# Kernel optimization log

Measured on AMD Instinct MI355X. Metric: run time of the kernel, lower is better.

The kernel has to match this reference:

```python
import jax, jax.numpy as jnp
import numpy as np

OBS, HOR, PD, HID, NH, PROTO = 8, 8, 128, 256, 8, 32
B, N = 8, 4096

def _gelu(x):
    return jax.nn.gelu(x, approximate=False)  # torch nn.GELU default is exact erf

def setup_inputs():
    key = jax.random.key(0)
    ks = iter(jax.random.split(key, 40))
    nrm = lambda shape, s=0.02: jax.random.normal(next(ks), shape, dtype=jnp.float32) * s
    return {
        'obs_points': jax.random.normal(next(ks), (B, N, OBS, 2), dtype=jnp.float32),
        'obs_vis': jax.random.randint(next(ks), (B, N, OBS), 0, 2).astype(bool),
        'rel_xy': jax.random.normal(next(ks), (B, N, 2), dtype=jnp.float32),
        'anchor_obs': jax.random.normal(next(ks), (B, OBS, 2), dtype=jnp.float32),
        'anchor_obs_vel': jax.random.normal(next(ks), (B, OBS, 2), dtype=jnp.float32),
        'semantic_feat': jax.random.normal(next(ks), (B, N, 10), dtype=jnp.float32),
        'ln_w': jnp.ones((OBS * 7,), jnp.float32),
        'ln_b': jnp.zeros((OBS * 7,), jnp.float32),
        'enc_w1': nrm((OBS * 7, PD)), 'enc_b1': jnp.zeros((PD,), jnp.float32),
        'enc_w2': nrm((PD, PD)), 'enc_b2': jnp.zeros((PD,), jnp.float32),
        'time_embed': nrm((HOR, HID)),
        'anchor_w': nrm((OBS * 4, HID)), 'anchor_b': jnp.zeros((HID,), jnp.float32),
        'query_w': nrm((PD, HID)), 'query_b': jnp.zeros((HID,), jnp.float32),
        'in_proj_w': nrm((HID, 3 * HID)), 'in_proj_b': jnp.zeros((3 * HID,), jnp.float32),
        'out_proj_w': nrm((HID, HID)), 'out_proj_b': jnp.zeros((HID,), jnp.float32),
        'ah_w': nrm((HID, 2)), 'ah_b': jnp.zeros((2,), jnp.float32),
        'rh_w1': nrm((HID + PD + 2, HID)), 'rh_b1': jnp.zeros((HID,), jnp.float32),
        'rh_w2': nrm((HID, 2)), 'rh_b2': jnp.zeros((2,), jnp.float32),
        'vh_w1': nrm((HID + PD, HID // 2)), 'vh_b1': jnp.zeros((HID // 2,), jnp.float32),
        'vh_w2': nrm((HID // 2, 1)), 'vh_b2': jnp.zeros((1,), jnp.float32),
        'sh_w': nrm((HID, PROTO)), 'sh_b': jnp.zeros((PROTO,), jnp.float32),
    }

def reference(obs_points, obs_vis, rel_xy, anchor_obs, anchor_obs_vel, semantic_feat,
              ln_w, ln_b, enc_w1, enc_b1, enc_w2, enc_b2, time_embed,
              anchor_w, anchor_b, query_w, query_b, in_proj_w, in_proj_b,
              out_proj_w, out_proj_b, ah_w, ah_b, rh_w1, rh_b1, rh_w2, rh_b2,
              vh_w1, vh_b1, vh_w2, vh_b2, sh_w, sh_b):
    del semantic_feat  # unused, matches original
    Bc, Nc, T, _ = obs_points.shape
    # ---- PointTraceEncoder ----
    vel = jnp.concatenate([jnp.zeros_like(obs_points[:, :, :1]),
                           obs_points[:, :, 1:] - obs_points[:, :, :-1]], axis=2)
    rel = jnp.broadcast_to(rel_xy[:, :, None, :], (Bc, Nc, T, 2))
    feat = jnp.concatenate([obs_points, vel, obs_vis.astype(jnp.float32)[..., None], rel],
                           axis=-1).reshape(Bc, Nc, T * 7)
    mu = feat.mean(-1, keepdims=True)
    var = ((feat - mu) ** 2).mean(-1, keepdims=True)
    x = (feat - mu) / jnp.sqrt(var + 1e-5) * ln_w + ln_b
    point_tokens = _gelu(_gelu(x @ enc_w1 + enc_b1) @ enc_w2 + enc_b2)  # [B,N,PD]
    # ---- queries / memory ----
    anchor_feat = jnp.concatenate([anchor_obs, anchor_obs_vel], -1).reshape(Bc, -1)
    tq = time_embed[None] + (anchor_feat @ anchor_w + anchor_b)[:, None]  # [B,HOR,HID]
    mem = point_tokens @ query_w + query_b  # [B,N,HID]
    # ---- multi-head cross attention ----
    D = tq.shape[-1]; dh = D // NH
    q = tq @ in_proj_w[:, :D] + in_proj_b[:D]
    k = mem @ in_proj_w[:, D:2 * D] + in_proj_b[D:2 * D]
    v = mem @ in_proj_w[:, 2 * D:] + in_proj_b[2 * D:]
    qh = q.reshape(Bc, -1, NH, dh).transpose(0, 2, 1, 3)
    kh = k.reshape(Bc, -1, NH, dh).transpose(0, 2, 1, 3)
    vh = v.reshape(Bc, -1, NH, dh).transpose(0, 2, 1, 3)
    attn = jax.nn.softmax(jnp.einsum('bhqd,bhkd->bhqk', qh, kh) / jnp.sqrt(jnp.float32(dh)), axis=-1)
    o = jnp.einsum('bhqk,bhkd->bhqd', attn, vh).transpose(0, 2, 1, 3).reshape(Bc, -1, D)
    future = o @ out_proj_w + out_proj_b  # [B,HOR,HID]
    # ---- heads ----
    last_anchor = anchor_obs[:, -1]
    anchor_delta = 0.1 * jnp.tanh(future @ ah_w + ah_b)
    anchor_pred = last_anchor[:, None] + jnp.cumsum(anchor_delta, axis=1)  # [B,HOR,2]
    Hq = future.shape[1]
    ft_e = jnp.broadcast_to(future[:, :, None, :], (Bc, Hq, Nc, D))
    pt_e = jnp.broadcast_to(point_tokens[:, None], (Bc, Hq, Nc, point_tokens.shape[-1]))
    rel_e = jnp.broadcast_to(rel_xy[:, None], (Bc, Hq, Nc, 2))
    per_point = jnp.concatenate([ft_e, pt_e, rel_e], axis=-1)  # [B,HOR,N,HID+PD+2]
    residual = 0.1 * jnp.tanh(_gelu(per_point @ rh_w1 + rh_b1) @ rh_w2 + rh_b2)
    pred_points = anchor_pred[:, :, None, :] + residual
    vis_logits = (_gelu(per_point[..., :-2] @ vh_w1 + vh_b1) @ vh_w2 + vh_b2)[..., 0]
    sem_logits = future @ sh_w + sh_b
    return (anchor_pred,
            pred_points.transpose(0, 2, 1, 3),   # [B,N,HOR,2]
            vis_logits.transpose(0, 2, 1),       # [B,N,HOR]
            sem_logits)                           # [B,HOR,PROTO]
```

## Files before the change

### kernel.cpp

```cpp
#include <hip/hip_runtime.h>
#include <math.h>

#define BB 8
#define NN 4096
#define TT 8
#define HORQ 8
#define PD 128
#define HID 256
#define NHD 8
#define DH 32
#define FE 56
#define NC2 16
#define CH2 256

typedef __attribute__((ext_vector_type(8))) short short8;
typedef __attribute__((ext_vector_type(4))) float floatx4;
typedef unsigned short ushort_t;

__device__ __forceinline__ float gelu_fast(float x) {
    float x2 = x * x;
    float y2 = x * fmaf(0.0713551f, x2, 1.5957691f);
    float e = __expf(y2);
    return x - x * __builtin_amdgcn_rcpf(1.f + e);
}

__device__ __forceinline__ float tanh_fast(float x) {
    float e = __expf(2.f * x);
    return 1.f - 2.f * __builtin_amdgcn_rcpf(1.f + e);
}

__device__ __forceinline__ ushort_t f2b(float x) {
    union { float f; unsigned u; } c; c.f = x;
    unsigned r = c.u + 0x7fffu + ((c.u >> 16) & 1u);
    return (ushort_t)(r >> 16);
}
__device__ __forceinline__ float b2f(unsigned hi) {
    union { unsigned u; float f; } c; c.u = hi;
    return c.f;
}

__global__ __launch_bounds__(256) void k_fuse(
    const float* __restrict__ qw, const float* __restrict__ qb,
    const float* __restrict__ ipw, const float* __restrict__ ipb,
    float* __restrict__ Wk, float* __restrict__ Wv,
    float* __restrict__ bk, float* __restrict__ bv)
{
    int j = threadIdx.x;
    int blk = blockIdx.x;
    if (blk < PD) {
        float sk = 0.f, sv = 0.f;
        for (int l = 0; l < HID; l++) {
            float w = qw[blk * HID + l];
            sk += w * ipw[l * 768 + 256 + j];
            sv += w * ipw[l * 768 + 512 + j];
        }
        Wk[blk * HID + j] = sk;
        Wv[blk * HID + j] = sv;
    } else {
        float sk = ipb[256 + j], sv = ipb[512 + j];
        for (int l = 0; l < HID; l++) {
            float w = qb[l];
            sk += w * ipw[l * 768 + 256 + j];
            sv += w * ipw[l * 768 + 512 + j];
        }
        bk[j] = sk;
        bv[j] = sv;
    }
}

__global__ __launch_bounds__(256) void k_prep(
    const float* __restrict__ Wk, const float* __restrict__ Wv,
    const float* __restrict__ rw1, const float* __restrict__ vw1,
    const float* __restrict__ w1, const float* __restrict__ w2,
    short* __restrict__ Wfrag, short* __restrict__ w1frag, short* __restrict__ w2frag)
{
    int tid = threadIdx.x;
    int blk = blockIdx.x;
    int ks = tid >> 6, lane = tid & 63;
    int quad = lane >> 4, c16 = lane & 15;
    if (blk < 56) {
        int nt = blk;
        int n = nt * 16 + c16;
        for (int j = 0; j < 8; j++) {
            int k = ks * 32 + quad * 8 + j;
            float v;
            if (n < 256)      v = Wk[k * HID + n];
            else if (n < 512) v = Wv[k * HID + (n - 256)];
            else if (n < 768) v = rw1[(256 + k) * HID + (n - 512)];
            else              v = vw1[(256 + k) * PD + (n - 768)];
            Wfrag[((nt * 4 + ks) * 64 + lane) * 8 + j] = (short)f2b(v);
        }
    } else if (blk < 64) {
        if (ks < 2) {
            int nt = blk - 56;
            int n = nt * 16 + c16;
            for (int j = 0; j < 8; j++) {
                int k = ks * 32 + quad * 8 + j;
                float v = (k < FE) ? w1[k * PD + n] : 0.f;
                w1frag[((nt * 2 + ks) * 64 + lane) * 8 + j] = (short)f2b(v);
            }
        }
    } else {
        int nt = blk - 64;
        int n = nt * 16 + c16;
        for (int j = 0; j < 8; j++) {
            int k = ks * 32 + quad * 8 + j;
            w2frag[((nt * 4 + ks) * 64 + lane) * 8 + j] = (short)f2b(w2[k * PD + n]);
        }
    }
}

#define U1_OFF 0
#define XNB_OFF 17408
#define PTB_OFF 26624
#define RXY_OFF 44032
#define MU_OFF 44544
#define RS_OFF 44800
#define SMEM_BYTES 45056

__global__ __launch_bounds__(256) void k_main(
    const float* __restrict__ obs, const int* __restrict__ vis,
    const float* __restrict__ rel,
    const float* __restrict__ lnw, const float* __restrict__ lnb,
    const float* __restrict__ b1, const float* __restrict__ b2,
    const short* __restrict__ Wfrag, const short* __restrict__ w1frag,
    const short* __restrict__ w2frag,
    const float* __restrict__ bk, const float* __restrict__ bv,
    const float* __restrict__ rw1,
    float* __restrict__ kb, float* __restrict__ vb,
    ushort_t* __restrict__ P1, ushort_t* __restrict__ P2)
{
    __shared__ __align__(16) char smem[SMEM_BYTES];
    float* xnf = (float*)(smem + U1_OFF);
    short* h1b = (short*)(smem + U1_OFF);
    short* xnb = (short*)(smem + XNB_OFF);
    short* ptb = (short*)(smem + PTB_OFF);
    float* rxyS = (float*)(smem + RXY_OFF);
    float* muS = (float*)(smem + MU_OFF);
    float* rsS = (float*)(smem + RS_OFF);

    int tid = threadIdx.x;
    int w = tid >> 6, lane = tid & 63;
    int quad = lane >> 4, c16 = lane & 15;
    int bn0 = blockIdx.x * 64;

    for (int idx = tid; idx < 64 * FE; idx += 256) {
        int p = idx / FE, e = idx - p * FE;
        int t = e / 7, c = e - t * 7;
        int bn = bn0 + p;
        float v;
        if (c < 2)       v = obs[(bn * TT + t) * 2 + c];
        else if (c < 4)  v = (t == 0) ? 0.f : (obs[(bn * TT + t) * 2 + (c - 2)] - obs[(bn * TT + t - 1) * 2 + (c - 2)]);
        else if (c == 4) v = (float)vis[bn * TT + t];
        else             v = rel[bn * 2 + (c - 5)];
        xnf[p * 57 + e] = v;
    }
    if (tid < 128) rxyS[tid] = rel[bn0 * 2 + tid];
    __syncthreads();

    if (tid < 64) {
        float s = 0.f, ss = 0.f;
        for (int e = 0; e < FE; e++) { float v = xnf[tid * 57 + e]; s += v; ss += v * v; }
        float mu = s * (1.f / FE);
        float var = ss * (1.f / FE) - mu * mu;
        muS[tid] = mu;
        rsS[tid] = rsqrtf(var + 1e-5f);
    }
    __syncthreads();

    for (int idx = tid; idx < 64 * 64; idx += 256) {
        int p = idx >> 6, e = idx & 63;
        float v = 0.f;
        if (e < FE) v = (xnf[p * 57 + e] - muS[p]) * rsS[p] * lnw[e] + lnb[e];
        xnb[p * 72 + e] = (short)f2b(v);
    }
    __syncthreads();

    {
        short8 af1[4][2];
        #pragma unroll
        for (int mt = 0; mt < 4; mt++)
            #pragma unroll
            for (int ks = 0; ks < 2; ks++)
                af1[mt][ks] = *(const short8*)(xnb + (mt * 16 + c16) * 72 + ks * 32 + quad * 8);
        #pragma unroll
        for (int ntl = 0; ntl < 2; ntl++) {
            int nt = w * 2 + ntl;
            short8 bf1[2];
            #pragma unroll
            for (int ks = 0; ks < 2; ks++)
                bf1[ks] = *(const short8*)(w1frag + ((nt * 2 + ks) * 64 + lane) * 8);
            int col = nt * 16 + c16;
            float bb = b1[col];
            #pragma unroll
            for (int mt = 0; mt < 4; mt++) {
                floatx4 acc = {0.f, 0.f, 0.f, 0.f};
                acc = __builtin_amdgcn_mfma_f32_16x16x32_bf16(af1[mt][0], bf1[0], acc, 0, 0, 0);
                acc = __builtin_amdgcn_mfma_f32_16x16x32_bf16(af1[mt][1], bf1[1], acc, 0, 0, 0);
                #pragma unroll
                for (int r = 0; r < 4; r++) {
                    int row = mt * 16 + quad * 4 + r;
                    h1b[row * 136 + col] = (short)f2b(gelu_fast(acc[r] + bb));
                }
            }
        }
    }
    __syncthreads();

    {
        short8 af2[4][4];
        #pragma unroll
        for (int mt = 0; mt < 4; mt++)
            #pragma unroll
            for (int ks = 0; ks < 4; ks++)
                af2[mt][ks] = *(const short8*)(h1b + (mt * 16 + c16) * 136 + ks * 32 + quad * 8);
        #pragma unroll
        for (int ntl = 0; ntl < 2; ntl++) {
            int nt = w * 2 + ntl;
            short8 bf2[4];
            #pragma unroll
            for (int ks = 0; ks < 4; ks++)
                bf2[ks] = *(const short8*)(w2frag + ((nt * 4 + ks) * 64 + lane) * 8);
            int col = nt * 16 + c16;
            float bb = b2[col];
            #pragma unroll
            for (int mt = 0; mt < 4; mt++) {
                floatx4 acc = {0.f, 0.f, 0.f, 0.f};
                #pragma unroll
                for (int ks = 0; ks < 4; ks++)
                    acc = __builtin_amdgcn_mfma_f32_16x16x32_bf16(af2[mt][ks], bf2[ks], acc, 0, 0, 0);
                #pragma unroll
                for (int r = 0; r < 4; r++) {
                    int row = mt * 16 + quad * 4 + r;
                    ptb[row * 136 + col] = (short)f2b(gelu_fast(acc[r] + bb));
                }
            }
        }
    }
    __syncthreads();

    {
        short8 af[4][4];
        #pragma unroll
        for (int mt = 0; mt < 4; mt++)
            #pragma unroll
            for (int ks = 0; ks < 4; ks++)
                af[mt][ks] = *(const short8*)(ptb + (mt * 16 + c16) * 136 + ks * 32 + quad * 8);
        for (int i = 0; i < 14; i++) {
            int nt = w + i * 4;
            short8 bf[4];
            #pragma unroll
            for (int ks = 0; ks < 4; ks++)
                bf[ks] = *(const short8*)(Wfrag + ((nt * 4 + ks) * 64 + lane) * 8);
            floatx4 acc[4];
            #pragma unroll
            for (int mt = 0; mt < 4; mt++) {
                acc[mt] = (floatx4){0.f, 0.f, 0.f, 0.f};
                #pragma unroll
                for (int ks = 0; ks < 4; ks++)
                    acc[mt] = __builtin_amdgcn_mfma_f32_16x16x32_bf16(af[mt][ks], bf[ks], acc[mt], 0, 0, 0);
            }
            int n = nt * 16 + c16;
            if (nt < 16) {
                float bb = bk[n];
                #pragma unroll
                for (int mt = 0; mt < 4; mt++)
                    #pragma unroll
                    for (int r = 0; r < 4; r++) {
                        int row = mt * 16 + quad * 4 + r;
                        kb[(size_t)(bn0 + row) * HID + n] = acc[mt][r] + bb;
                    }
            } else if (nt < 32) {
                int j = n - 256;
                float bb = bv[j];
                #pragma unroll
                for (int mt = 0; mt < 4; mt++)
                    #pragma unroll
                    for (int r = 0; r < 4; r++) {
                        int row = mt * 16 + quad * 4 + r;
                        vb[(size_t)(bn0 + row) * HID + j] = acc[mt][r] + bb;
                    }
            } else if (nt < 48) {
                int j = n - 512;
                float wr0 = rw1[384 * HID + j], wr1 = rw1[385 * HID + j];
                #pragma unroll
                for (int mt = 0; mt < 4; mt++)
                    #pragma unroll
                    for (int r = 0; r < 4; r++) {
                        int row = mt * 16 + quad * 4 + r;
                        P1[(size_t)(bn0 + row) * HID + j] =
                            f2b(acc[mt][r] + rxyS[row * 2] * wr0 + rxyS[row * 2 + 1] * wr1);
                    }
            } else {
                int j = n - 768;
                #pragma unroll
                for (int mt = 0; mt < 4; mt++)
                    #pragma unroll
                    for (int r = 0; r < 4; r++) {
                        int row = mt * 16 + quad * 4 + r;
                        P2[(size_t)(bn0 + row) * PD + j] = f2b(acc[mt][r]);
                    }
            }
        }
    }
}

__global__ __launch_bounds__(256) void k_tq(
    const float* __restrict__ aobs, const float* __restrict__ avel,
    const float* __restrict__ te, const float* __restrict__ aw, const float* __restrict__ ab,
    const float* __restrict__ ipw, const float* __restrict__ ipb,
    float* __restrict__ qb_)
{
    __shared__ float af[32];
    __shared__ float tq[HID];
    int tid = threadIdx.x;
    int b = blockIdx.x >> 3, h = blockIdx.x & 7;
    if (tid < 32) {
        int t = tid >> 2, m = tid & 3;
        af[tid] = (m < 2) ? aobs[(b * TT + t) * 2 + m] : avel[(b * TT + t) * 2 + (m - 2)];
    }
    __syncthreads();
    float s = te[h * HID + tid] + ab[tid];
    for (int i = 0; i < 32; i++) s += af[i] * aw[i * HID + tid];
    tq[tid] = s;
    __syncthreads();
    float qv = ipb[tid];
    for (int i = 0; i < HID; i++) qv += tq[i] * ipw[i * 768 + tid];
    qb_[(size_t)blockIdx.x * HID + tid] = qv;
}

__global__ __launch_bounds__(256) void k_att(
    const float* __restrict__ qbuf, const float* __restrict__ kb, const float* __restrict__ vbuf,
    float* __restrict__ pm, float* __restrict__ pl, float* __restrict__ po)
{
    __shared__ float qs[8][DH];
    __shared__ float sc[8][CH2];
    __shared__ float pos[8][8][DH];
    int tid = threadIdx.x;
    int bidx = blockIdx.x;
    int c = bidx & (NC2 - 1);
    int head = (bidx >> 4) & 7;
    int b = bidx >> 7;
    qs[tid >> 5][tid & 31] = qbuf[(size_t)(b * HORQ + (tid >> 5)) * HID + head * DH + (tid & 31)];
    __syncthreads();
    const float scale = 0.17677669529663688110f;
    {
        int nn = tid;
        int n = c * CH2 + nn;
        const float* kp = kb + (size_t)(b * NN + n) * HID + head * DH;
        float kr[DH];
        #pragma unroll
        for (int u = 0; u < DH; u += 4) {
            float4 f = *reinterpret_cast<const float4*>(kp + u);
            kr[u] = f.x; kr[u + 1] = f.y; kr[u + 2] = f.z; kr[u + 3] = f.w;
        }
        #pragma unroll
        for (int qq = 0; qq < 8; qq++) {
            float s = 0.f;
            #pragma unroll
            for (int d = 0; d < DH; d++) s += qs[qq][d] * kr[d];
            sc[qq][nn] = s * scale;
        }
    }
    __syncthreads();
    int qq = tid >> 5, r = tid & 31;
    float mx = -1e30f;
    #pragma unroll
    for (int nn = r; nn < CH2; nn += 32) mx = fmaxf(mx, sc[qq][nn]);
    #pragma unroll
    for (int m = 16; m; m >>= 1) mx = fmaxf(mx, __shfl_xor(mx, m, 32));
    float sum = 0.f;
    #pragma unroll
    for (int nn = r; nn < CH2; nn += 32) { float e = __expf(sc[qq][nn] - mx); sc[qq][nn] = e; sum += e; }
    #pragma unroll
    for (int m = 16; m; m >>= 1) sum += __shfl_xor(sum, m, 32);
    if (r == 0) { pm[bidx * 8 + qq] = mx; pl[bidx * 8 + qq] = sum; }
    __syncthreads();
    {
        int g = tid >> 5, d = tid & 31;
        float oacc[8];
        #pragma unroll
        for (int q2 = 0; q2 < 8; q2++) oacc[q2] = 0.f;
        const float* vp = vbuf + ((size_t)(b * NN + c * CH2 + g * 32)) * HID + head * DH + d;
        for (int i = 0; i < 32; i++) {
            float v = vp[(size_t)i * HID];
            int nn = g * 32 + i;
            #pragma unroll
            for (int q2 = 0; q2 < 8; q2++) oacc[q2] += sc[q2][nn] * v;
        }
        #pragma unroll
        for (int q2 = 0; q2 < 8; q2++) pos[g][q2][d] = oacc[q2];
    }
    __syncthreads();
    {
        int q2 = tid >> 5, d = tid & 31;
        float o = 0.f;
        #pragma unroll
        for (int gg = 0; gg < 8; gg++) o += pos[gg][q2][d];
        po[(size_t)(bidx * 8 + q2) * DH + d] = o;
    }
}

__global__ __launch_bounds__(256) void k_attc(
    const float* __restrict__ pm, const float* __restrict__ pl, const float* __restrict__ po,
    float* __restrict__ ob)
{
    int tid = threadIdx.x;
    int bh = blockIdx.x;
    int b = bh >> 3, head = bh & 7;
    int qq = tid >> 5, d = tid & 31;
    float M = -1e30f;
    for (int c = 0; c < NC2; c++) M = fmaxf(M, pm[(bh * NC2 + c) * 8 + qq]);
    float L = 0.f, o = 0.f;
    for (int c = 0; c < NC2; c++) {
        float w = __expf(pm[(bh * NC2 + c) * 8 + qq] - M);
        L += w * pl[(bh * NC2 + c) * 8 + qq];
        o += w * po[(size_t)((bh * NC2 + c) * 8 + qq) * DH + d];
    }
    ob[(size_t)(b * HORQ + qq) * HID + head * DH + d] = o / L;
}

__global__ __launch_bounds__(256) void k_fut(
    const float* __restrict__ ob, const float* __restrict__ opw, const float* __restrict__ opb,
    const float* __restrict__ rw1, const float* __restrict__ rb1,
    const float* __restrict__ vw1, const float* __restrict__ vb1,
    const float* __restrict__ shw, const float* __restrict__ shb,
    const float* __restrict__ ahw, const float* __restrict__ ahb,
    float* __restrict__ F1, float* __restrict__ F2, float* __restrict__ dl, float* __restrict__ sem)
{
    __shared__ float orow[HID], fut[HID];
    int tid = threadIdx.x;
    int bh = blockIdx.x;
    orow[tid] = ob[(size_t)bh * HID + tid];
    __syncthreads();
    float s = opb[tid];
    for (int i = 0; i < HID; i++) s += orow[i] * opw[i * HID + tid];
    fut[tid] = s;
    __syncthreads();
    float f1 = rb1[tid];
    for (int i = 0; i < HID; i++) f1 += fut[i] * rw1[i * HID + tid];
    F1[(size_t)bh * HID + tid] = f1;
    if (tid < PD) {
        float f2 = vb1[tid];
        for (int i = 0; i < HID; i++) f2 += fut[i] * vw1[i * PD + tid];
        F2[(size_t)bh * PD + tid] = f2;
    }
    if (tid < 32) {
        float s3 = shb[tid];
        for (int i = 0; i < HID; i++) s3 += fut[i] * shw[i * 32 + tid];
        sem[bh * 32 + tid] = s3;
    }
    if (tid < 2) {
        float a = ahb[tid];
        for (int i = 0; i < HID; i++) a += fut[i] * ahw[i * 2 + tid];
        dl[bh * 2 + tid] = 0.1f * tanhf(a);
    }
}

__global__ void k_cum(const float* __restrict__ aobs, const float* __restrict__ dl, float* __restrict__ out0)
{
    int tid = threadIdx.x;
    if (tid < 16) {
        int b = tid >> 1, c = tid & 1;
        float acc = aobs[(b * TT + 7) * 2 + c];
        for (int h = 0; h < HORQ; h++) {
            acc += dl[(b * HORQ + h) * 2 + c];
            out0[(b * HORQ + h) * 2 + c] = acc;
        }
    }
}

__global__ __launch_bounds__(256) void k_fin(
    const float* __restrict__ F1, const float* __restrict__ F2,
    const ushort_t* __restrict__ P1, const ushort_t* __restrict__ P2,
    const float* __restrict__ rw2, const float* __restrict__ rb2,
    const float* __restrict__ vw2, const float* __restrict__ vb2,
    const float* __restrict__ ap,
    float* __restrict__ out1, float* __restrict__ out2)
{
    int tile = blockIdx.x >> 1;
    int hh = blockIdx.x & 1;
    int h0 = hh * 4;
    int bn = tile * 256 + threadIdx.x;
    int b = bn >> 12;

    const uint4* p1v = (const uint4*)(P1 + (size_t)bn * HID);
    const uint4* p2v = (const uint4*)(P2 + (size_t)bn * PD);
    const float* f1base = F1 + (size_t)(b * HORQ + h0) * HID;
    const float* f2base = F2 + (size_t)(b * HORQ + h0) * PD;

    float acc0[4], acc1[4], accv[4];
    #pragma unroll
    for (int hi = 0; hi < 4; hi++) { acc0[hi] = 0.f; acc1[hi] = 0.f; accv[hi] = 0.f; }

    for (int c = 0; c < 32; c++) {
        uint4 q = p1v[c];
        unsigned wd[4] = {q.x, q.y, q.z, q.w};
        float p1f[8];
        #pragma unroll
        for (int u = 0; u < 4; u++) {
            p1f[2 * u]     = b2f(wd[u] << 16);
            p1f[2 * u + 1] = b2f(wd[u] & 0xffff0000u);
        }
        float w0[8], w1[8];
        #pragma unroll
        for (int u = 0; u < 8; u++) {
            int j = c * 8 + u;
            w0[u] = rw2[j * 2];
            w1[u] = rw2[j * 2 + 1];
        }
        #pragma unroll
        for (int hi = 0; hi < 4; hi++) {
            const float* f1p = f1base + hi * HID + c * 8;
            #pragma unroll
            for (int u = 0; u < 8; u++) {
                float g = gelu_fast(f1p[u] + p1f[u]);
                acc0[hi] += g * w0[u];
                acc1[hi] += g * w1[u];
            }
        }
    }
    for (int c = 0; c < 16; c++) {
        uint4 q = p2v[c];
        unsigned wd[4] = {q.x, q.y, q.z, q.w};
        float p2f[8];
        #pragma unroll
        for (int u = 0; u < 4; u++) {
            p2f[2 * u]     = b2f(wd[u] << 16);
            p2f[2 * u + 1] = b2f(wd[u] & 0xffff0000u);
        }
        float wv[8];
        #pragma unroll
        for (int u = 0; u < 8; u++) wv[u] = vw2[c * 8 + u];
        #pragma unroll
        for (int hi = 0; hi < 4; hi++) {
            const float* f2p = f2base + hi * PD + c * 8;
            #pragma unroll
            for (int u = 0; u < 8; u++) {
                float g = gelu_fast(f2p[u] + p2f[u]);
                accv[hi] += g * wv[u];
            }
        }
    }

    float rb20 = rb2[0], rb21 = rb2[1], vb20 = vb2[0];
    float o1[8], o2[4];
    #pragma unroll
    for (int hi = 0; hi < 4; hi++) {
        int h = h0 + hi;
        float rx = 0.1f * tanh_fast(acc0[hi] + rb20);
        float ry = 0.1f * tanh_fast(acc1[hi] + rb21);
        o1[2 * hi]     = ap[(b * HORQ + h) * 2 + 0] + rx;
        o1[2 * hi + 1] = ap[(b * HORQ + h) * 2 + 1] + ry;
        o2[hi] = accv[hi] + vb20;
    }
    float4* o1p = (float4*)(out1 + ((size_t)bn * HORQ + h0) * 2);
    o1p[0] = make_float4(o1[0], o1[1], o1[2], o1[3]);
    o1p[1] = make_float4(o1[4], o1[5], o1[6], o1[7]);
    *(float4*)(out2 + (size_t)bn * HORQ + h0) = make_float4(o2[0], o2[1], o2[2], o2[3]);
}

extern "C" void kernel_launch(void* const* d_in, const int* in_sizes, int n_in,
                              void* d_out, int out_size, void* d_ws, size_t ws_size,
                              hipStream_t stream)
{
    const float* obs  = (const float*)d_in[0];
    const int*   vis  = (const int*)d_in[1];
    const float* rel  = (const float*)d_in[2];
    const float* aobs = (const float*)d_in[3];
    const float* avel = (const float*)d_in[4];
    const float* lnw = (const float*)d_in[6];
    const float* lnb = (const float*)d_in[7];
    const float* ew1 = (const float*)d_in[8];
    const float* eb1 = (const float*)d_in[9];
    const float* ew2 = (const float*)d_in[10];
    const float* eb2 = (const float*)d_in[11];
    const float* te  = (const float*)d_in[12];
    const float* aw  = (const float*)d_in[13];
    const float* ab  = (const float*)d_in[14];
    const float* qw  = (const float*)d_in[15];
    const float* qbias = (const float*)d_in[16];
    const float* ipw = (const float*)d_in[17];
    const float* ipb = (const float*)d_in[18];
    const float* opw = (const float*)d_in[19];
    const float* opb = (const float*)d_in[20];
    const float* ahw = (const float*)d_in[21];
    const float* ahb = (const float*)d_in[22];
    const float* rw1 = (const float*)d_in[23];
    const float* rb1 = (const float*)d_in[24];
    const float* rw2 = (const float*)d_in[25];
    const float* rb2 = (const float*)d_in[26];
    const float* vw1 = (const float*)d_in[27];
    const float* vb1 = (const float*)d_in[28];
    const float* vw2 = (const float*)d_in[29];
    const float* vb2 = (const float*)d_in[30];
    const float* shw = (const float*)d_in[31];
    const float* shb = (const float*)d_in[32];

    float* W = (float*)d_ws;
    size_t o = 0;
    float* Wk  = W + o; o += (size_t)PD * HID;
    float* Wv  = W + o; o += (size_t)PD * HID;
    float* bk  = W + o; o += HID;
    float* bv  = W + o; o += HID;
    float* qb_ = W + o; o += (size_t)BB * HORQ * HID;
    float* F1  = W + o; o += (size_t)BB * HORQ * HID;
    float* F2  = W + o; o += (size_t)BB * HORQ * PD;
    float* dl  = W + o; o += (size_t)BB * HORQ * 2;
    float* ob  = W + o; o += (size_t)BB * HORQ * HID;
    float* pm  = W + o; o += (size_t)BB * NHD * NC2 * 8;
    float* pl  = W + o; o += (size_t)BB * NHD * NC2 * 8;
    float* po  = W + o; o += (size_t)BB * NHD * NC2 * 8 * DH;
    float* kb  = W + o; o += (size_t)BB * NN * HID;
    float* vbuf= W + o; o += (size_t)BB * NN * HID;
    ushort_t* P1 = (ushort_t*)(W + o); o += (size_t)BB * NN * HID / 2;
    ushort_t* P2 = (ushort_t*)(W + o); o += (size_t)BB * NN * PD / 2;
    short* Sf = (short*)(W + o);
    short* Wfrag  = Sf;
    short* w1frag = Sf + 114688;
    short* w2frag = Sf + 114688 + 8192;

    float* out0 = (float*)d_out;
    float* out1 = out0 + BB * HORQ * 2;
    float* out2 = out1 + (size_t)BB * NN * HORQ * 2;
    float* out3 = out2 + (size_t)BB * NN * HORQ;

    k_fuse<<<PD + 1, 256, 0, stream>>>(qw, qbias, ipw, ipb, Wk, Wv, bk, bv);
    k_prep<<<72, 256, 0, stream>>>(Wk, Wv, rw1, vw1, ew1, ew2, Wfrag, w1frag, w2frag);
    k_main<<<BB * NN / 64, 256, 0, stream>>>(obs, vis, rel, lnw, lnb, eb1, eb2,
                                             Wfrag, w1frag, w2frag, bk, bv, rw1,
                                             kb, vbuf, P1, P2);
    k_tq<<<BB * HORQ, 256, 0, stream>>>(aobs, avel, te, aw, ab, ipw, ipb, qb_);
    k_att<<<BB * NHD * NC2, 256, 0, stream>>>(qb_, kb, vbuf, pm, pl, po);
    k_attc<<<BB * NHD, 256, 0, stream>>>(pm, pl, po, ob);
    k_fut<<<BB * HORQ, 256, 0, stream>>>(ob, opw, opb, rw1, rb1, vw1, vb1, shw, shb, ahw, ahb,
                                         F1, F2, dl, out3);
    k_cum<<<1, 64, 0, stream>>>(aobs, dl, out0);
    k_fin<<<(BB * NN / 256) * 2, 256, 0, stream>>>(F1, F2, P1, P2, rw2, rb2, vw2, vb2,
                                                   out0, out1, out2);
}
```

Before: 290.3 us.

## Store K/V in bf16, merge small kernels, and restructure final head kernel

K and V projections are now written as bf16 instead of fp32, halving the traffic that k_main writes and k_att reads. The query-prep kernel is folded into k_prep as extra blocks, and the attention-combine kernel is merged into the future-projection kernel, which removes two launches and the ob buffer. k_fin is rewritten so each 32-lane group handles one point, looping over horizons with shuffle reductions instead of one thread per point. The bf16 K/V adds rounding error to the attention scores and weighted sums.

New measurement: 273.8 us. -5.7%, faster.

```diff
diff --git a/kernel.cpp b/kernel.cpp
--- a/kernel.cpp
+++ b/kernel.cpp
@@ -72,8 +72,14 @@
     const float* __restrict__ Wk, const float* __restrict__ Wv,
     const float* __restrict__ rw1, const float* __restrict__ vw1,
     const float* __restrict__ w1, const float* __restrict__ w2,
-    short* __restrict__ Wfrag, short* __restrict__ w1frag, short* __restrict__ w2frag)
-{
+    const float* __restrict__ aobs, const float* __restrict__ avel,
+    const float* __restrict__ te, const float* __restrict__ aw, const float* __restrict__ ab,
+    const float* __restrict__ ipw, const float* __restrict__ ipb,
+    short* __restrict__ Wfrag, short* __restrict__ w1frag, short* __restrict__ w2frag,
+    float* __restrict__ qb_)
+{
+    __shared__ float af[32];
+    __shared__ float tqs[HID];
     int tid = threadIdx.x;
     int blk = blockIdx.x;
     int ks = tid >> 6, lane = tid & 63;
@@ -100,13 +106,28 @@
                 w1frag[((nt * 2 + ks) * 64 + lane) * 8 + j] = (short)f2b(v);
             }
         }
-    } else {
+    } else if (blk < 72) {
         int nt = blk - 64;
         int n = nt * 16 + c16;
         for (int j = 0; j < 8; j++) {
             int k = ks * 32 + quad * 8 + j;
             w2frag[((nt * 4 + ks) * 64 + lane) * 8 + j] = (short)f2b(w2[k * PD + n]);
         }
+    } else {
+        int bh = blk - 72;
+        int b = bh >> 3, h = bh & 7;
+        if (tid < 32) {
+            int t = tid >> 2, m = tid & 3;
+            af[tid] = (m < 2) ? aobs[(b * TT + t) * 2 + m] : avel[(b * TT + t) * 2 + (m - 2)];
+        }
+        __syncthreads();
+        float s = te[h * HID + tid] + ab[tid];
+        for (int i = 0; i < 32; i++) s += af[i] * aw[i * HID + tid];
+        tqs[tid] = s;
+        __syncthreads();
+        float qv = ipb[tid];
+        for (int i = 0; i < HID; i++) qv += tqs[i] * ipw[i * 768 + tid];
+        qb_[(size_t)bh * HID + tid] = qv;
     }
 }
 
@@ -127,7 +148,7 @@
     const short* __restrict__ w2frag,
     const float* __restrict__ bk, const float* __restrict__ bv,
     const float* __restrict__ rw1,
-    float* __restrict__ kb, float* __restrict__ vb,
+    ushort_t* __restrict__ kb, ushort_t* __restrict__ vb,
     ushort_t* __restrict__ P1, ushort_t* __restrict__ P2)
 {
     __shared__ __align__(16) char smem[SMEM_BYTES];
@@ -268,7 +289,7 @@
                     #pragma unroll
                     for (int r = 0; r < 4; r++) {
                         int row = mt * 16 + quad * 4 + r;
-                        kb[(size_t)(bn0 + row) * HID + n] = acc[mt][r] + bb;
+                        kb[(size_t)(bn0 + row) * HID + n] = f2b(acc[mt][r] + bb);
                     }
             } else if (nt < 32) {
                 int j = n - 256;
@@ -278,7 +299,7 @@
                     #pragma unroll
                     for (int r = 0; r < 4; r++) {
                         int row = mt * 16 + quad * 4 + r;
-                        vb[(size_t)(bn0 + row) * HID + j] = acc[mt][r] + bb;
+                        vb[(size_t)(bn0 + row) * HID + j] = f2b(acc[mt][r] + bb);
                     }
             } else if (nt < 48) {
                 int j = n - 512;
@@ -305,32 +326,8 @@
     }
 }
 
-__global__ __launch_bounds__(256) void k_tq(
-    const float* __restrict__ aobs, const float* __restrict__ avel,
-    const float* __restrict__ te, const float* __restrict__ aw, const float* __restrict__ ab,
-    const float* __restrict__ ipw, const float* __restrict__ ipb,
-    float* __restrict__ qb_)
-{
-    __shared__ float af[32];
-    __shared__ float tq[HID];
-    int tid = threadIdx.x;
-    int b = blockIdx.x >> 3, h = blockIdx.x & 7;
-    if (tid < 32) {
-        int t = tid >> 2, m = tid & 3;
-        af[tid] = (m < 2) ? aobs[(b * TT + t) * 2 + m] : avel[(b * TT + t) * 2 + (m - 2)];
-    }
-    __syncthreads();
-    float s = te[h * HID + tid] + ab[tid];
-    for (int i = 0; i < 32; i++) s += af[i] * aw[i * HID + tid];
-    tq[tid] = s;
-    __syncthreads();
-    float qv = ipb[tid];
-    for (int i = 0; i < HID; i++) qv += tq[i] * ipw[i * 768 + tid];
-    qb_[(size_t)blockIdx.x * HID + tid] = qv;
-}
-
 __global__ __launch_bounds__(256) void k_att(
-    const float* __restrict__ qbuf, const float* __restrict__ kb, const float* __restrict__ vbuf,
+    const float* __restrict__ qbuf, const ushort_t* __restrict__ kb, const ushort_t* __restrict__ vbuf,
     float* __restrict__ pm, float* __restrict__ pl, float* __restrict__ po)
 {
     __shared__ float qs[8][DH];
@@ -347,12 +344,17 @@
     {
         int nn = tid;
         int n = c * CH2 + nn;
-        const float* kp = kb + (size_t)(b * NN + n) * HID + head * DH;
+        const ushort_t* kp = kb + (size_t)(b * NN + n) * HID + head * DH;
         float kr[DH];
         #pragma unroll
-        for (int u = 0; u < DH; u += 4) {
-            float4 f = *reinterpret_cast<const float4*>(kp + u);
-            kr[u] = f.x; kr[u + 1] = f.y; kr[u + 2] = f.z; kr[u + 3] = f.w;
+        for (int u = 0; u < 4; u++) {
+            uint4 q = *reinterpret_cast<const uint4*>(kp + u * 8);
+            unsigned wd[4] = {q.x, q.y, q.z, q.w};
+            #pragma unroll
+            for (int t2 = 0; t2 < 4; t2++) {
+                kr[u * 8 + 2 * t2]     = b2f(wd[t2] << 16);
+                kr[u * 8 + 2 * t2 + 1] = b2f(wd[t2] & 0xffff0000u);
+            }
         }
         #pragma unroll
         for (int qq = 0; qq < 8; qq++) {
@@ -381,9 +383,9 @@
         float oacc[8];
         #pragma unroll
         for (int q2 = 0; q2 < 8; q2++) oacc[q2] = 0.f;
-        const float* vp = vbuf + ((size_t)(b * NN + c * CH2 + g * 32)) * HID + head * DH + d;
+        const ushort_t* vp = vbuf + ((size_t)(b * NN + c * CH2 + g * 32)) * HID + head * DH + d;
         for (int i = 0; i < 32; i++) {
-            float v = vp[(size_t)i * HID];
+            float v = b2f(((unsigned)vp[(size_t)i * HID]) << 16);
             int nn = g * 32 + i;
             #pragma unroll
             for (int q2 = 0; q2 < 8; q2++) oacc[q2] += sc[q2][nn] * v;
@@ -401,27 +403,9 @@
     }
 }
 
-__global__ __launch_bounds__(256) void k_attc(
+__global__ __launch_bounds__(256) void k_attfut(
     const float* __restrict__ pm, const float* __restrict__ pl, const float* __restrict__ po,
-    float* __restrict__ ob)
-{
-    int tid = threadIdx.x;
-    int bh = blockIdx.x;
-    int b = bh >> 3, head = bh & 7;
-    int qq = tid >> 5, d = tid & 31;
-    float M = -1e30f;
-    for (int c = 0; c < NC2; c++) M = fmaxf(M, pm[(bh * NC2 + c) * 8 + qq]);
-    float L = 0.f, o = 0.f;
-    for (int c = 0; c < NC2; c++) {
-        float w = __expf(pm[(bh * NC2 + c) * 8 + qq] - M);
-        L += w * pl[(bh * NC2 + c) * 8 + qq];
-        o += w * po[(size_t)((bh * NC2 + c) * 8 + qq) * DH + d];
-    }
-    ob[(size_t)(b * HORQ + qq) * HID + head * DH + d] = o / L;
-}
-
-__global__ __launch_bounds__(256) void k_fut(
-    const float* __restrict__ ob, const float* __restrict__ opw, const float* __restrict__ opb,
+    const float* __restrict__ opw, const float* __restrict__ opb,
     const float* __restrict__ rw1, const float* __restrict__ rb1,
     const float* __restrict__ vw1, const float* __restrict__ vb1,
     const float* __restrict__ shw, const float* __restrict__ shb,
@@ -430,13 +414,28 @@
 {
     __shared__ float orow[HID], fut[HID];
     int tid = threadIdx.x;
-    int bh = blockIdx.x;
-    orow[tid] = ob[(size_t)bh * HID + tid];
+    int b = blockIdx.x >> 3, qq = blockIdx.x & 7;
+    {
+        int head = tid >> 5, d = tid & 31;
+        int base = b * 1024 + head * 128 + qq;
+        float M = -1e30f;
+        #pragma unroll
+        for (int c = 0; c < NC2; c++) M = fmaxf(M, pm[base + c * 8]);
+        float L = 0.f, o = 0.f;
+        #pragma unroll
+        for (int c = 0; c < NC2; c++) {
+            float wgt = __expf(pm[base + c * 8] - M);
+            L += wgt * pl[base + c * 8];
+            o += wgt * po[(size_t)(base + c * 8) * DH + d];
+        }
+        orow[head * DH + d] = o / L;
+    }
     __syncthreads();
     float s = opb[tid];
     for (int i = 0; i < HID; i++) s += orow[i] * opw[i * HID + tid];
     fut[tid] = s;
     __syncthreads();
+    int bh = b * HORQ + qq;
     float f1 = rb1[tid];
     for (int i = 0; i < HID; i++) f1 += fut[i] * rw1[i * HID + tid];
     F1[(size_t)bh * HID + tid] = f1;
@@ -478,86 +477,76 @@
     const float* __restrict__ ap,
     float* __restrict__ out1, float* __restrict__ out2)
 {
-    int tile = blockIdx.x >> 1;
-    int hh = blockIdx.x & 1;
-    int h0 = hh * 4;
-    int bn = tile * 256 + threadIdx.x;
+    int tid = threadIdx.x;
+    int sub = tid >> 5;
+    int l = tid & 31;
+    int bn = blockIdx.x * 8 + sub;
     int b = bn >> 12;
 
-    const uint4* p1v = (const uint4*)(P1 + (size_t)bn * HID);
-    const uint4* p2v = (const uint4*)(P2 + (size_t)bn * PD);
-    const float* f1base = F1 + (size_t)(b * HORQ + h0) * HID;
-    const float* f2base = F2 + (size_t)(b * HORQ + h0) * PD;
-
-    float acc0[4], acc1[4], accv[4];
-    #pragma unroll
-    for (int hi = 0; hi < 4; hi++) { acc0[hi] = 0.f; acc1[hi] = 0.f; accv[hi] = 0.f; }
-
-    for (int c = 0; c < 32; c++) {
-        uint4 q = p1v[c];
-        unsigned wd[4] = {q.x, q.y, q.z, q.w};
-        float p1f[8];
+    uint4 q1 = *(const uint4*)(P1 + (size_t)bn * HID + l * 8);
+    float p1f[8];
+    {
+        unsigned wd[4] = {q1.x, q1.y, q1.z, q1.w};
         #pragma unroll
         for (int u = 0; u < 4; u++) {
             p1f[2 * u]     = b2f(wd[u] << 16);
             p1f[2 * u + 1] = b2f(wd[u] & 0xffff0000u);
         }
-        float w0[8], w1[8];
+    }
+    float w0[8], w1[8];
+    {
+        const float4* rwp = (const float4*)(rw2 + l * 16);
+        #pragma unroll
+        for (int u = 0; u < 4; u++) {
+            float4 r = rwp[u];
+            w0[2 * u] = r.x; w1[2 * u] = r.y;
+            w0[2 * u + 1] = r.z; w1[2 * u + 1] = r.w;
+        }
+    }
+    float p2f[4];
+    {
+        uint2 q2 = *(const uint2*)(P2 + (size_t)bn * PD + l * 4);
+        p2f[0] = b2f(q2.x << 16); p2f[1] = b2f(q2.x & 0xffff0000u);
+        p2f[2] = b2f(q2.y << 16); p2f[3] = b2f(q2.y & 0xffff0000u);
+    }
+    float4 wvv = *(const float4*)(vw2 + l * 4);
+    float wv[4] = {wvv.x, wvv.y, wvv.z, wvv.w};
+
+    float rb20 = rb2[0], rb21 = rb2[1], vb20 = vb2[0];
+    for (int h = 0; h < HORQ; h++) {
+        const float* f1p = F1 + (size_t)(b * HORQ + h) * HID + l * 8;
+        float4 fa = *(const float4*)f1p;
+        float4 fb = *(const float4*)(f1p + 4);
+        float f1r[8] = {fa.x, fa.y, fa.z, fa.w, fb.x, fb.y, fb.z, fb.w};
+        float4 f2v = *(const float4*)(F2 + (size_t)(b * HORQ + h) * PD + l * 4);
+        float f2r[4] = {f2v.x, f2v.y, f2v.z, f2v.w};
+        float s0 = 0.f, s1 = 0.f, sv = 0.f;
         #pragma unroll
         for (int u = 0; u < 8; u++) {
-            int j = c * 8 + u;
-            w0[u] = rw2[j * 2];
-            w1[u] = rw2[j * 2 + 1];
-        }
-        #pragma unroll
-        for (int hi = 0; hi < 4; hi++) {
-            const float* f1p = f1base + hi * HID + c * 8;
-            #pragma unroll
-            for (int u = 0; u < 8; u++) {
-                float g = gelu_fast(f1p[u] + p1f[u]);
-                acc0[hi] += g * w0[u];
-                acc1[hi] += g * w1[u];
-            }
-        }
-    }
-    for (int c = 0; c < 16; c++) {
-        uint4 q = p2v[c];
-        unsigned wd[4] = {q.x, q.y, q.z, q.w};
-        float p2f[8];
+            float g = gelu_fast(f1r[u] + p1f[u]);
+            s0 += g * w0[u];
+            s1 += g * w1[u];
+        }
         #pragma unroll
         for (int u = 0; u < 4; u++) {
-            p2f[2 * u]     = b2f(wd[u] << 16);
-            p2f[2 * u + 1] = b2f(wd[u] & 0xffff0000u);
-        }
-        float wv[8];
-        #pragma unroll
-        for (int u = 0; u < 8; u++) wv[u] = vw2[c * 8 + u];
-        #pragma unroll
-        for (int hi = 0; hi < 4; hi++) {
-            const float* f2p = f2base + hi * PD + c * 8;
-            #pragma unroll
-            for (int u = 0; u < 8; u++) {
-                float g = gelu_fast(f2p[u] + p2f[u]);
-                accv[hi] += g * wv[u];
-            }
-        }
-    }
-
-    float rb20 = rb2[0], rb21 = rb2[1], vb20 = vb2[0];
-    float o1[8], o2[4];
-    #pragma unroll
-    for (int hi = 0; hi < 4; hi++) {
-        int h = h0 + hi;
-        float rx = 0.1f * tanh_fast(acc0[hi] + rb20);
-        float ry = 0.1f * tanh_fast(acc1[hi] + rb21);
-        o1[2 * hi]     = ap[(b * HORQ + h) * 2 + 0] + rx;
-        o1[2 * hi + 1] = ap[(b * HORQ + h) * 2 + 1] + ry;
-        o2[hi] = accv[hi] + vb20;
-    }
-    float4* o1p = (float4*)(out1 + ((size_t)bn * HORQ + h0) * 2);
-    o1p[0] = make_float4(o1[0], o1[1], o1[2], o1[3]);
-    o1p[1] = make_float4(o1[4], o1[5], o1[6], o1[7]);
-    *(float4*)(out2 + (size_t)bn * HORQ + h0) = make_float4(o2[0], o2[1], o2[2], o2[3]);
+            float g = gelu_fast(f2r[u] + p2f[u]);
+            sv += g * wv[u];
+        }
+        #pragma unroll
+        for (int m = 16; m; m >>= 1) {
+            s0 += __shfl_xor(s0, m, 32);
+            s1 += __shfl_xor(s1, m, 32);
+            sv += __shfl_xor(sv, m, 32);
+        }
+        if (l == 0) {
+            float rx = 0.1f * tanh_fast(s0 + rb20);
+            float ry = 0.1f * tanh_fast(s1 + rb21);
+            int bh = b * HORQ + h;
+            out1[((size_t)bn * HORQ + h) * 2 + 0] = ap[bh * 2 + 0] + rx;
+            out1[((size_t)bn * HORQ + h) * 2 + 1] = ap[bh * 2 + 1] + ry;
+            out2[(size_t)bn * HORQ + h] = sv + vb20;
+        }
+    }
 }
 
 extern "C" void kernel_launch(void* const* d_in, const int* in_sizes, int n_in,
@@ -607,14 +596,13 @@
     float* F1  = W + o; o += (size_t)BB * HORQ * HID;
     float* F2  = W + o; o += (size_t)BB * HORQ * PD;
     float* dl  = W + o; o += (size_t)BB * HORQ * 2;
-    float* ob  = W + o; o += (size_t)BB * HORQ * HID;
     float* pm  = W + o; o += (size_t)BB * NHD * NC2 * 8;
     float* pl  = W + o; o += (size_t)BB * NHD * NC2 * 8;
     float* po  = W + o; o += (size_t)BB * NHD * NC2 * 8 * DH;
-    float* kb  = W + o; o += (size_t)BB * NN * HID;
-    float* vbuf= W + o; o += (size_t)BB * NN * HID;
-    ushort_t* P1 = (ushort_t*)(W + o); o += (size_t)BB * NN * HID / 2;
-    ushort_t* P2 = (ushort_t*)(W + o); o += (size_t)BB * NN * PD / 2;
+    ushort_t* kb   = (ushort_t*)(W + o); o += (size_t)BB * NN * HID / 2;
+    ushort_t* vbuf = (ushort_t*)(W + o); o += (size_t)BB * NN * HID / 2;
+    ushort_t* P1   = (ushort_t*)(W + o); o += (size_t)BB * NN * HID / 2;
+    ushort_t* P2   = (ushort_t*)(W + o); o += (size_t)BB * NN * PD / 2;
     short* Sf = (short*)(W + o);
     short* Wfrag  = Sf;
     short* w1frag = Sf + 114688;
@@ -626,16 +614,16 @@
     float* out3 = out2 + (size_t)BB * NN * HORQ;
 
     k_fuse<<<PD + 1, 256, 0, stream>>>(qw, qbias, ipw, ipb, Wk, Wv, bk, bv);
-    k_prep<<<72, 256, 0, stream>>>(Wk, Wv, rw1, vw1, ew1, ew2, Wfrag, w1frag, w2frag);
+    k_prep<<<72 + 64, 256, 0, stream>>>(Wk, Wv, rw1, vw1, ew1, ew2,
+                                        aobs, avel, te, aw, ab, ipw, ipb,
+                                        Wfrag, w1frag, w2frag, qb_);
     k_main<<<BB * NN / 64, 256, 0, stream>>>(obs, vis, rel, lnw, lnb, eb1, eb2,
                                              Wfrag, w1frag, w2frag, bk, bv, rw1,
                                              kb, vbuf, P1, P2);
-    k_tq<<<BB * HORQ, 256, 0, stream>>>(aobs, avel, te, aw, ab, ipw, ipb, qb_);
     k_att<<<BB * NHD * NC2, 256, 0, stream>>>(qb_, kb, vbuf, pm, pl, po);
-    k_attc<<<BB * NHD, 256, 0, stream>>>(pm, pl, po, ob);
-    k_fut<<<BB * HORQ, 256, 0, stream>>>(ob, opw, opb, rw1, rb1, vw1, vb1, shw, shb, ahw, ahb,
-                                         F1, F2, dl, out3);
+    k_attfut<<<BB * HORQ, 256, 0, stream>>>(pm, pl, po, opw, opb, rw1, rb1, vw1, vb1,
+                                            shw, shb, ahw, ahb, F1, F2, dl, out3);
     k_cum<<<1, 64, 0, stream>>>(aobs, dl, out0);
-    k_fin<<<(BB * NN / 256) * 2, 256, 0, stream>>>(F1, F2, P1, P2, rw2, rb2, vw2, vb2,
-                                                   out0, out1, out2);
-}
+    k_fin<<<BB * NN / 8, 256, 0, stream>>>(F1, F2, P1, P2, rw2, rb2, vw2, vb2,
+                                           out0, out1, out2);
+}
```
